# Kernel tuning notes

Measured on AMD Instinct MI355X. Metric: run time of the kernel, lower is better.

## Reference

```python
import jax, jax.numpy as jnp
import numpy as np

EPS = 1e-5

def conv3d(x, w):
    # x: [B,C,D,H,W], w: [O,I,3,3,3], stride 1, padding 1 (size preserving)
    return jax.lax.conv_general_dilated(
        x, w, window_strides=(1, 1, 1),
        padding=((1, 1), (1, 1), (1, 1)),
        dimension_numbers=('NCDHW', 'OIDHW', 'NCDHW'))

def deconv3d(x, w):
    # ConvTranspose3d(k=3, s=1, p=1) == conv3d with spatially flipped kernel, in/out swapped
    # torch ConvTranspose3d weight layout: [in, out, kD, kH, kW]
    wc = jnp.flip(w, axis=(2, 3, 4)).transpose(1, 0, 2, 3, 4)
    return conv3d(x, wc)

def batchnorm(x, bn):
    # bn: [4, C] rows = (gamma, beta, running_mean, running_var); inference mode
    g, b, m, v = bn[0], bn[1], bn[2], bn[3]
    scale = g * jax.lax.rsqrt(v + EPS)
    shift = b - m * scale
    return x * scale[None, :, None, None, None] + shift[None, :, None, None, None]

def qrnn_scan(Z, F, reverse):
    # gated linear recurrence h_t = f_t*h_{t-1} + (1-f_t)*z_t over depth axis (dim 2)
    Zs = jnp.moveaxis(Z, 2, 0)  # [D,B,C,H,W]
    Fs = jnp.moveaxis(F, 2, 0)
    def step(h, zf):
        z, f = zf
        h = f * h + (1.0 - f) * z
        return h, h
    h0 = jnp.zeros_like(Zs[0])  # h=None in torch == h=0 since f*0 vanishes
    _, hs = jax.lax.scan(step, h0, (Zs, Fs), reverse=reverse)
    return jnp.moveaxis(hs, 0, 2)

def qrnn_layer(x, w, bn, hidden, reverse, upsample, transpose):
    if upsample:
        # nn.Upsample(scale_factor=(1,2,2)) nearest
        x = jnp.repeat(jnp.repeat(x, 2, axis=3), 2, axis=4)
    g = deconv3d(x, w) if transpose else conv3d(x, w)
    g = batchnorm(g, bn)
    Z, F = g[:, :hidden], g[:, hidden:]
    return qrnn_scan(jnp.tanh(Z), jax.nn.sigmoid(F), reverse)

def setup_inputs():
    key = jax.random.key(0)
    ks = jax.random.split(key, 12)
    B, D = 4, 31
    x = jax.random.normal(ks[0], (B, 64, D, 32, 32), jnp.float32)
    xs2 = jax.random.normal(ks[1], (B, 32, D, 64, 64), jnp.float32)
    xs1 = jax.random.normal(ks[2], (B, 32, D, 64, 64), jnp.float32)
    xs0 = jax.random.normal(ks[3], (B, 16, D, 128, 128), jnp.float32)
    def wconv(k, shape):
        fan_in = shape[1] * 27
        return jax.random.normal(k, shape, jnp.float32) / np.float32(np.sqrt(fan_in))
    # layer0: UpsampleConv3d 64 -> 32 hidden (gates 64): Conv3d weight [64,64,3,3,3]
    w0 = wconv(ks[4], (64, 64, 3, 3, 3))
    # layer1: DeConv3D 32 -> 32 hidden (gates 64): ConvTranspose weight [in=32,out=64,3,3,3]
    w1 = wconv(ks[5], (32, 64, 3, 3, 3))
    # layer2: UpsampleConv3d 32 -> 16 hidden (gates 32): Conv3d weight [32,32,3,3,3]
    w2 = wconv(ks[6], (32, 32, 3, 3, 3))
    # layer3: DeConv3D 16 -> 16 hidden (gates 32): ConvTranspose weight [16,32,3,3,3]
    w3 = wconv(ks[7], (16, 32, 3, 3, 3))
    def mkbn(k, c):
        k1, k2, k3, k4 = jax.random.split(k, 4)
        return jnp.stack([
            jax.random.uniform(k1, (c,), jnp.float32, 0.5, 1.5),   # gamma
            jax.random.normal(k2, (c,), jnp.float32) * 0.1,        # beta
            jax.random.normal(k3, (c,), jnp.float32) * 0.1,        # running mean
            jax.random.uniform(k4, (c,), jnp.float32, 0.5, 1.5)])  # running var
    bn0 = mkbn(ks[8], 64)
    bn1 = mkbn(ks[9], 64)
    bn2 = mkbn(ks[10], 32)
    bn3 = mkbn(ks[11], 32)
    return dict(x=x, xs0=xs0, xs1=xs1, xs2=xs2,
                w0=w0, w1=w1, w2=w2, w3=w3,
                bn0=bn0, bn1=bn1, bn2=bn2, bn3=bn3)

def reference(x, xs0, xs1, xs2, w0, w1, w2, w3, bn0, bn1, bn2, bn3):
    # QRNN3DDecoder.forward with has_ad=True, reverse=False; scan direction alternates.
    # xs are popped last-first: xs2, xs1, xs0.
    h = qrnn_layer(x, w0, bn0, 32, False, True, False)          # upsample conv -> [B,32,D,64,64]
    h = qrnn_layer(h + xs2, w1, bn1, 32, True, False, True)     # deconv        -> [B,32,D,64,64]
    h = qrnn_layer(h + xs1, w2, bn2, 16, False, True, False)    # upsample conv -> [B,16,D,128,128]
    h = qrnn_layer(h + xs0, w3, bn3, 16, True, False, True)     # deconv        -> [B,16,D,128,128]
    return h
```

## Files before the change

### kernel.cpp

```cpp
#include <hip/hip_runtime.h>
#include <math.h>

#define BB 4
#define DD 31

typedef _Float16 half8 __attribute__((ext_vector_type(8)));
typedef float f32x4 __attribute__((ext_vector_type(4)));

__device__ __forceinline__ int swz(int b) { return b ^ (((b >> 7) & 7) << 4); }
__device__ __forceinline__ half8 ldswz(const _Float16* lin, int byteoff) {
    return *(const half8*)((const char*)lin + swz(byteoff));
}
__device__ __forceinline__ void stswz(_Float16* lin, int byteoff, half8 v) {
    *(half8*)((char*)lin + swz(byteoff)) = v;
}
__device__ __forceinline__ float fast_tanh(float y) {
    float e = __expf(2.f * y);
    return 1.f - 2.f * __builtin_amdgcn_rcpf(e + 1.f);
}
__device__ __forceinline__ float fast_sigmoid(float y) {
    return __builtin_amdgcn_rcpf(1.f + __expf(-y));
}


__global__ void bnprep(const float* __restrict__ bn, int C, float* __restrict__ sh) {
    int c = threadIdx.x;
    if (c >= C) return;
    float g = bn[c], b = bn[C + c], m = bn[2 * C + c], v = bn[3 * C + c];
    sh[c] = b - m * (g * rsqrtf(v + 1e-5f));
}

__global__ void wprepA(const float* __restrict__ src, const float* __restrict__ bn,
                       _Float16* __restrict__ dst, int CIN, int COUT, int KS, int tr) {
    int idx = blockIdx.x * 256 + threadIdx.x;
    int total = KS * 32 * COUT;
    if (idx >= total) return;
    int ki = idx % 32;
    int co = (idx / 32) % COUT;
    int ko = idx / (32 * COUT);
    int k = ko * 32 + ki;
    float v = 0.f;
    if (k < 27 * CIN) {
        int tap = k / CIN, ci = k % CIN;
        v = tr ? src[((size_t)ci * COUT + co) * 27 + (26 - tap)]
               : src[((size_t)co * CIN + ci) * 27 + tap];
        v *= bn[co] * rsqrtf(bn[3 * COUT + co] + 1e-5f);
    }
    dst[((size_t)ko * COUT + co) * 32 + ki] = (_Float16)v;
}

__global__ void wprepC(const float* __restrict__ src, const float* __restrict__ bn,
                       _Float16* __restrict__ dst, int CIN, int COUT, int KS, int tr) {
    int idx = blockIdx.x * 256 + threadIdx.x;
    int total = KS * 1024;
    if (idx >= total) return;
    int ki = idx & 31;
    int c16 = (idx >> 5) & 15;
    int n = (idx >> 9) & 1;
    int ko = idx >> 10;
    int co = n * (COUT / 2) + c16;
    int k = ko * 32 + ki;
    float v = 0.f;
    if (k < 27 * CIN) {
        int tap = k / CIN, ci = k % CIN;
        v = tr ? src[((size_t)ci * COUT + co) * 27 + (26 - tap)]
               : src[((size_t)co * CIN + ci) * 27 + tap];
        v *= bn[co] * rsqrtf(bn[3 * COUT + co] + 1e-5f);
    }
    dst[idx] = (_Float16)v;
}

__global__ void wprep_upA(const float* __restrict__ src, const float* __restrict__ bn,
                          _Float16* __restrict__ dst, int CIN, int COUT) {
    const int KS = 12 * CIN / 32;
    int idx = blockIdx.x * 256 + threadIdx.x;
    int total = 4 * KS * 32 * COUT;
    if (idx >= total) return;
    int ki = idx % 32;
    int co = (idx / 32) % COUT;
    int ko = (idx / (32 * COUT)) % KS;
    int par = idx / (32 * COUT * KS);
    int k = ko * 32 + ki;
    int ci = k % CIN, tap = k / CIN;
    int kd = tap >> 2, ih = (tap >> 1) & 1, iw = tap & 1;
    int ph = par >> 1, pw = par & 1;
    const float c[2][2][3] = {{{1, 0, 0}, {0, 1, 1}}, {{1, 1, 0}, {0, 0, 1}}};
    float v = 0.f;
    for (int kh = 0; kh < 3; ++kh)
        for (int kw = 0; kw < 3; ++kw)
            v += c[ph][ih][kh] * c[pw][iw][kw] *
                 src[((size_t)co * CIN + ci) * 27 + kd * 9 + kh * 3 + kw];
    v *= bn[co] * rsqrtf(bn[3 * COUT + co] + 1e-5f);
    dst[(((size_t)par * KS + ko) * COUT + co) * 32 + ki] = (_Float16)v;
}

__global__ void wprep_upB(const float* __restrict__ src, const float* __restrict__ bn,
                          _Float16* __restrict__ dst, int CIN, int COUT, int KS) {
    int idx = blockIdx.x * 256 + threadIdx.x;
    int total = 4 * KS * 1024;
    if (idx >= total) return;
    int ki = idx & 31;
    int c16 = (idx >> 5) & 15;
    int n = (idx >> 9) & 1;
    int ko = (idx >> 10) % KS;
    int par = idx / (KS * 1024);
    int co = n * (COUT / 2) + c16;
    int k = ko * 32 + ki;
    int ci = k % CIN, tap = k / CIN;
    int kd = tap >> 2, ih = (tap >> 1) & 1, iw = tap & 1;
    int ph = par >> 1, pw = par & 1;
    const float c[2][2][3] = {{{1, 0, 0}, {0, 1, 1}}, {{1, 1, 0}, {0, 0, 1}}};
    float v = 0.f;
    for (int kh = 0; kh < 3; ++kh)
        for (int kw = 0; kw < 3; ++kw)
            v += c[ph][ih][kh] * c[pw][iw][kw] *
                 src[((size_t)co * CIN + ci) * 27 + kd * 9 + kh * 3 + kw];
    v *= bn[co] * rsqrtf(bn[3 * COUT + co] + 1e-5f);
    dst[idx] = (_Float16)v;
}

__global__ __launch_bounds__(256) void xconv(const float* __restrict__ src,
                                             _Float16* __restrict__ dst) {
    int idx = blockIdx.x * 256 + threadIdx.x;
    if (idx >= 4 * 31 * 1024 * 8) return;
    int cb = idx & 7;
    int pos = (idx >> 3) & 1023;
    int bd = idx >> 13;
    int d = bd % 31, b = bd / 31;
    half8 v;
#pragma unroll
    for (int j = 0; j < 8; ++j)
        v[j] = (_Float16)src[(((size_t)b * 64 + cb * 8 + j) * 31 + d) * 1024 + pos];
    *(half8*)(dst + ((size_t)bd * 1024 + pos) * 64 + cb * 8) = v;
}

template <int C, int HW>
__global__ __launch_bounds__(256) void xst(const float* __restrict__ src,
                                           _Float16* __restrict__ dst) {
    int hw = blockIdx.x * 256 + threadIdx.x;
    int bd = blockIdx.y;
    int d = bd % DD, b = bd / DD;
    _Float16 tmp[C];
#pragma unroll
    for (int c = 0; c < C; ++c)
        tmp[c] = (_Float16)src[((size_t)(b * C + c) * DD + d) * HW + hw];
#pragma unroll
    for (int c8 = 0; c8 < C / 8; ++c8)
        *(half8*)(dst + ((size_t)bd * HW + hw) * C + c8 * 8) = *(half8*)(tmp + c8 * 8);
}

template <int CIN, int COUT, int S, int MINW>
__global__ __launch_bounds__(256, MINW) void conv_up(
    const _Float16* __restrict__ inp,
    const _Float16* __restrict__ wqu,
    const float* __restrict__ bnsh,
    _Float16* __restrict__ gout) {

    constexpr int SIN = S / 2;
    constexpr int KS = 12 * CIN / 32;
    constexpr int NCB = COUT / 16;
    constexpr int NC8 = CIN / 8;
    constexpr int IH = 6, IW = 18;
    constexpr int PATCH = 3 * IH * IW;

    __shared__ __align__(16) _Float16 lin[PATCH * CIN];

    const int tid = threadIdx.x;
    const int lane = tid & 63;
    const int wv = tid >> 6;
    const int col = lane & 15;
    const int grp = lane >> 4;
    const int ph = wv >> 1, pw = wv & 1;

    const int bwp = blockIdx.x * 16;
    const int bhp = blockIdx.y * 4;
    const int bz = blockIdx.z;
    const int d = bz % DD;

    for (int idx = tid; idx < PATCH * NC8; idx += 256) {
        int c8 = idx % NC8;
        int pos = idx / NC8;
        int iwp = pos % IW, t = pos / IW;
        int ihp = t % IH, kd = t / IH;
        int dz = d + kd - 1, gh = bhp - 1 + ihp, gw = bwp - 1 + iwp;
        half8 v = {0, 0, 0, 0, 0, 0, 0, 0};
        if ((unsigned)dz < (unsigned)DD && (unsigned)gh < (unsigned)SIN &&
            (unsigned)gw < (unsigned)SIN)
            v = *(const half8*)(inp +
                (((size_t)(bz + kd - 1) * SIN + gh) * SIN + gw) * CIN + c8 * 8);
        *(half8*)((char*)lin + swz((pos * CIN + c8 * 8) * 2)) = v;
    }
    __syncthreads();

    f32x4 acc[4][NCB];
#pragma unroll
    for (int f = 0; f < 4; ++f)
#pragma unroll
        for (int n = 0; n < NCB; ++n) acc[f][n] = {0.f, 0.f, 0.f, 0.f};

    const _Float16* wqp = wqu + (size_t)(ph * 2 + pw) * KS * COUT * 32;

#pragma unroll
    for (int ko = 0; ko < KS; ++ko) {
        int tap = (ko * 32) / CIN;
        int ci = (ko * 32) % CIN + grp * 8;
        int kd = tap >> 2, ih = (tap >> 1) & 1, iwk = tap & 1;

        int lcol = col + iwk + pw;
        int r0 = ih + ph;
        int cb = ((kd * IH + r0) * IW + lcol) * CIN + ci;
        half8 a[4];
#pragma unroll
        for (int f = 0; f < 4; ++f)
            a[f] = ldswz(lin, (cb + f * IW * CIN) * 2);

        half8 bfr[NCB];
#pragma unroll
        for (int n = 0; n < NCB; ++n)
            bfr[n] = *(const half8*)(wqp + ((ko * COUT + n * 16 + col) * 32 + grp * 8));
#pragma unroll
        for (int f = 0; f < 4; ++f)
#pragma unroll
            for (int n = 0; n < NCB; ++n)
                acc[f][n] = __builtin_amdgcn_mfma_f32_16x16x32_f16(a[f], bfr[n],
                                                                   acc[f][n], 0, 0, 0);
    }

    const size_t obase = (size_t)bz * S * S * COUT;
#pragma unroll
    for (int n = 0; n < NCB; ++n) {
        int co = n * 16 + col;
        float sh = bnsh[co];
#pragma unroll
        for (int f = 0; f < 4; ++f) {
            int h = 2 * (bhp + f) + ph;
#pragma unroll
            for (int r = 0; r < 4; ++r) {
                int w = 2 * (bwp + grp * 4 + r) + pw;
                float y = acc[f][n][r] + sh;
                float v = (n < NCB / 2) ? fast_tanh(y) : fast_sigmoid(y);
                gout[obase + ((size_t)h * S + w) * COUT + co] = (_Float16)v;
            }
        }
    }
}

template <int CIN, int COUT, int S, int KSTEPS>
__global__ __launch_bounds__(256, 2) void conv_mfma(
    const _Float16* __restrict__ inp,
    const _Float16* __restrict__ wq,
    const float* __restrict__ bnsh,
    _Float16* __restrict__ gout) {

    constexpr int IH = 18;
    constexpr int IW = 18;
    constexpr int NCB = COUT / 16;
    constexpr int NC8 = CIN / 8;
    constexpr int PATCH = 3 * IH * IW;

    __shared__ __align__(16) _Float16 lin[PATCH * CIN];

    const int tid = threadIdx.x;
    const int lane = tid & 63;
    const int wv = tid >> 6;
    const int col = lane & 15;
    const int grp = lane >> 4;

    const int w0 = blockIdx.x * 16;
    const int h0 = blockIdx.y * 16;
    const int bz = blockIdx.z;
    const int d = bz % DD;

    const int ibh = h0 - 1;
    const int ibw = w0 - 1;

    for (int idx = tid; idx < PATCH * NC8; idx += 256) {
        int c8 = idx % NC8;
        int pos = idx / NC8;
        int iw = pos % IW, t = pos / IW;
        int ih = t % IH, kd = t / IH;
        int dz = d + kd - 1, gh = ibh + ih, gw = ibw + iw;
        half8 v = {0, 0, 0, 0, 0, 0, 0, 0};
        if ((unsigned)dz < (unsigned)DD && (unsigned)gh < (unsigned)S &&
            (unsigned)gw < (unsigned)S)
            v = *(const half8*)(inp +
                (((size_t)(bz + kd - 1) * S + gh) * S + gw) * CIN + c8 * 8);
        *(half8*)((char*)lin + swz((pos * CIN + c8 * 8) * 2)) = v;
    }
    __syncthreads();

    f32x4 acc[4][NCB];
#pragma unroll
    for (int f = 0; f < 4; ++f)
#pragma unroll
        for (int n = 0; n < NCB; ++n) acc[f][n] = {0.f, 0.f, 0.f, 0.f};

#pragma unroll
    for (int ko = 0; ko < KSTEPS; ++ko) {
        int tap = (ko * 32) / CIN;
        int kd = tap / 9, kh = (tap / 3) % 3, kw = tap % 3;
        int ci = (ko * 32) % CIN + grp * 8;

        half8 a[4];
        int iw = col + kw;
        int cb = ((kd * IH + wv * 4 + kh) * IW + iw) * CIN + ci;
#pragma unroll
        for (int f = 0; f < 4; ++f)
            a[f] = ldswz(lin, (cb + f * IW * CIN) * 2);

        half8 bfr[NCB];
#pragma unroll
        for (int n = 0; n < NCB; ++n)
            bfr[n] = *(const half8*)(wq + ((ko * COUT + n * 16 + col) * 32 + grp * 8));
#pragma unroll
        for (int f = 0; f < 4; ++f)
#pragma unroll
            for (int n = 0; n < NCB; ++n)
                acc[f][n] = __builtin_amdgcn_mfma_f32_16x16x32_f16(a[f], bfr[n],
                                                                   acc[f][n], 0, 0, 0);
    }

    const size_t obase = (size_t)bz * S * S * COUT;
#pragma unroll
    for (int n = 0; n < NCB; ++n) {
        int co = n * 16 + col;
        float sh = bnsh[co];
#pragma unroll
        for (int f = 0; f < 4; ++f) {
            int h = h0 + wv * 4 + f;
#pragma unroll
            for (int r = 0; r < 4; ++r) {
                int w = w0 + grp * 4 + r;
                float y = acc[f][n][r] + sh;
                float v = (n < NCB / 2) ? fast_tanh(y) : fast_sigmoid(y);
                gout[obase + ((size_t)h * S + w) * COUT + co] = (_Float16)v;
            }
        }
    }
}

template <int H, int HW>
__global__ __launch_bounds__(256) void qscan(
    const _Float16* __restrict__ g, const float* __restrict__ xs,
    _Float16* __restrict__ hout, int rev) {
    constexpr int NCB = H / 8;
    int idx = blockIdx.x * 256 + threadIdx.x;
    if (idx >= BB * HW * NCB) return;
    int cb = idx % NCB;
    int hw = (idx / NCB) % HW;
    int b = idx / (NCB * HW);
    int c0 = cb * 8;

    float h[8];
#pragma unroll
    for (int j = 0; j < 8; ++j) h[j] = 0.f;

    for (int t = 0; t < DD; ++t) {
        int d = rev ? (DD - 1 - t) : t;
        const _Float16* gp = g + ((size_t)(b * DD + d) * HW + hw) * (2 * H);
        half8 z8 = *(const half8*)(gp + c0);
        half8 f8 = *(const half8*)(gp + H + c0);
        half8 o;
#pragma unroll
        for (int j = 0; j < 8; ++j) {
            float fv = (float)f8[j];
            h[j] = fv * h[j] + (1.f - fv) * (float)z8[j];
            o[j] = (_Float16)(h[j] + xs[(((size_t)b * H + c0 + j) * DD + d) * HW + hw]);
        }
        *(half8*)(hout + ((size_t)(b * DD + d) * HW + hw) * H + c0) = o;
    }
}

template <int CIN, int S, int HID, int KS, int REV, int LAST>
__global__ __launch_bounds__(256, 2) void fconv_up1(
    const _Float16* __restrict__ inp,
    const _Float16* __restrict__ wq,
    const float* __restrict__ bnsh,
    const _Float16* __restrict__ xs,
    _Float16* __restrict__ hout,
    float* __restrict__ fout) {

    constexpr int SIN = S / 2;
    constexpr int IW = 18;
    constexpr int IHP = 6;
    constexpr int NC8 = CIN / 8;
    constexpr int P8 = IHP * IW * NC8;
    constexpr int NST = (P8 + 255) / 256;
    constexpr int PLANEB = IHP * IW * CIN * 2;
    constexpr int LWB = 3 * PLANEB;
    constexpr int WH = KS * 1024;

    __shared__ __align__(16) _Float16 lds[(LWB / 2) + WH];

    const int tid = threadIdx.x;
    const int lane = tid & 63;
    const int wv = tid >> 6;
    const int col = lane & 15;
    const int grp = lane >> 4;

    const int bwp = blockIdx.x * 16;
    const int bhp = blockIdx.y * 4;
    const int par = blockIdx.z & 3;
    const int b = blockIdx.z >> 2;
    const int ph = par >> 1, pw = par & 1;
    const size_t bbase = (size_t)b * DD;

    const float shz = bnsh[col];
    const float shf = bnsh[HID + col];
    const int hc = col;
    const _Float16* wqb = wq + (size_t)par * KS * 1024;

    auto stage_now = [&](int dz) {
        int slot = (dz + 33) % 3;
        for (int idx = tid; idx < P8; idx += 256) {
            int c8 = idx % NC8;
            int pos = idx / NC8;
            int ih = pos / IW, iw = pos % IW;
            int gh = bhp - 1 + ih, gw = bwp - 1 + iw;
            half8 v = {0, 0, 0, 0, 0, 0, 0, 0};
            if ((unsigned)dz < (unsigned)DD && (unsigned)gh < (unsigned)SIN &&
                (unsigned)gw < (unsigned)SIN)
                v = *(const half8*)(inp + (((bbase + dz) * SIN + gh) * SIN + gw) * CIN + c8 * 8);
            stswz(lds, slot * PLANEB + (pos * CIN + c8 * 8) * 2, v);
        }
    };

    constexpr int dir = REV ? -1 : 1;
    const int d0 = REV ? DD - 1 : 0;
    stage_now(d0 - dir);
    stage_now(d0);
    stage_now(d0 + dir);
    for (int i = tid; i < WH / 8; i += 256) {
        half8 v = *(const half8*)(wqb + i * 8);
        stswz(lds, LWB + i * 16, v);
    }
    __syncthreads();

    float hst[4];
#pragma unroll
    for (int r = 0; r < 4; ++r) hst[r] = 0.f;

    for (int t = 0; t < DD; ++t) {
        const int d = d0 + dir * t;
        const int dzl = d + 2 * dir;
        const int sm = (d - 1 + 33) % 3;
        const int s0 = (d + 33) % 3;
        const int sp = (d + 1 + 33) % 3;
        const int scommit = REV ? sp : sm;

        half8 sv[NST];
#pragma unroll
        for (int i = 0; i < NST; ++i) {
            int idx = tid + i * 256;
            half8 v = {0, 0, 0, 0, 0, 0, 0, 0};
            if (idx < P8) {
                int c8 = idx % NC8;
                int pos = idx / NC8;
                int ih = pos / IW, iw = pos % IW;
                int gh = bhp - 1 + ih, gw = bwp - 1 + iw;
                if ((unsigned)dzl < (unsigned)DD && (unsigned)gh < (unsigned)SIN &&
                    (unsigned)gw < (unsigned)SIN)
                    v = *(const half8*)(inp +
                        (((bbase + dzl) * SIN + gh) * SIN + gw) * CIN + c8 * 8);
            }
            sv[i] = v;
        }

        f32x4 accz = {0.f, 0.f, 0.f, 0.f};
        f32x4 accf = {0.f, 0.f, 0.f, 0.f};
#pragma unroll
        for (int ko = 0; ko < KS; ++ko) {
            int tap = (ko * 32) / CIN;
            int ci = (ko * 32) % CIN + grp * 8;
            int kd = tap >> 2, ihh = (tap >> 1) & 1, iwk = tap & 1;
            int slot = kd == 0 ? sm : (kd == 1 ? s0 : sp);
            int lcol = col + iwk + pw;
            int row = wv + ihh + ph;
            half8 a = ldswz(lds, slot * PLANEB + ((row * IW + lcol) * CIN + ci) * 2);
            half8 bf0 = ldswz(lds, LWB + (ko * 1024 + col * 32 + grp * 8) * 2);
            half8 bf1 = ldswz(lds, LWB + (ko * 1024 + 512 + col * 32 + grp * 8) * 2);
            accz = __builtin_amdgcn_mfma_f32_16x16x32_f16(a, bf0, accz, 0, 0, 0);
            accf = __builtin_amdgcn_mfma_f32_16x16x32_f16(a, bf1, accf, 0, 0, 0);
        }

        __syncthreads();
#pragma unroll
        for (int i = 0; i < NST; ++i) {
            int idx = tid + i * 256;
            if (idx < P8) {
                int c8 = idx % NC8;
                int pos = idx / NC8;
                stswz(lds, scommit * PLANEB + (pos * CIN + c8 * 8) * 2, sv[i]);
            }
        }

        int h = 2 * (bhp + wv) + ph;
#pragma unroll
        for (int r = 0; r < 4; ++r) {
            int w = 2 * (bwp + grp * 4 + r) + pw;
            size_t sp2 = (size_t)h * S + w;
            float z = fast_tanh(accz[r] + shz);
            float fg = fast_sigmoid(accf[r] + shf);
            hst[r] = fg * hst[r] + (1.f - fg) * z;
            if (LAST) {
                fout[(((size_t)b * HID + hc) * DD + d) * ((size_t)S * S) + sp2] = hst[r];
            } else {
                float xv = (float)xs[((bbase + d) * ((size_t)S * S) + sp2) * HID + hc];
                hout[((bbase + d) * ((size_t)S * S) + sp2) * HID + hc] =
                    (_Float16)(hst[r] + xv);
            }
        }
        __syncthreads();
    }
}

template <int CIN, int S, int HID, int KS, int NF, int REV>
__global__ __launch_bounds__(256, 2) void fconv3(
    const _Float16* __restrict__ inp,
    const _Float16* __restrict__ wq,
    const float* __restrict__ bnsh,
    float* __restrict__ fout) {

    constexpr int IW = 18;
    constexpr int TH = 4 * NF;
    constexpr int IHP = TH + 2;
    constexpr int NC8 = CIN / 8;
    constexpr int P8 = IHP * IW * NC8;
    constexpr int NST = (P8 + 255) / 256;
    constexpr int PLANEB = IHP * IW * CIN * 2;
    constexpr int LWB = 3 * PLANEB;
    constexpr int WH = KS * 1024;

    __shared__ __align__(16) _Float16 lds[(LWB / 2) + WH];

    const int tid = threadIdx.x;
    const int lane = tid & 63;
    const int wv = tid >> 6;
    const int col = lane & 15;
    const int grp = lane >> 4;

    const int w0 = blockIdx.x * 16;
    const int h0 = blockIdx.y * TH;
    const int b = blockIdx.z;
    const size_t bbase = (size_t)b * DD;

    const float shz = bnsh[col];
    const float shf = bnsh[HID + col];
    const int hc = col;

    auto stage_now = [&](int dz) {
        int slot = (dz + 33) % 3;
        for (int idx = tid; idx < P8; idx += 256) {
            int c8 = idx % NC8;
            int pos = idx / NC8;
            int ih = pos / IW, iw = pos % IW;
            int gh = h0 - 1 + ih, gw = w0 - 1 + iw;
            half8 v = {0, 0, 0, 0, 0, 0, 0, 0};
            if ((unsigned)dz < (unsigned)DD && (unsigned)gh < (unsigned)S &&
                (unsigned)gw < (unsigned)S)
                v = *(const half8*)(inp + (((bbase + dz) * S + gh) * S + gw) * CIN + c8 * 8);
            stswz(lds, slot * PLANEB + (pos * CIN + c8 * 8) * 2, v);
        }
    };

    constexpr int dir = REV ? -1 : 1;
    const int d0 = REV ? DD - 1 : 0;
    stage_now(d0 - dir);
    stage_now(d0);
    stage_now(d0 + dir);
    for (int i = tid; i < WH / 8; i += 256) {
        half8 v = *(const half8*)(wq + i * 8);
        stswz(lds, LWB + i * 16, v);
    }
    __syncthreads();

    float hst[NF][4];
#pragma unroll
    for (int f = 0; f < NF; ++f)
#pragma unroll
        for (int r = 0; r < 4; ++r) hst[f][r] = 0.f;

    for (int t = 0; t < DD; ++t) {
        const int d = d0 + dir * t;
        const int dzl = d + 2 * dir;
        const int sm = (d - 1 + 33) % 3;
        const int s0 = (d + 33) % 3;
        const int sp = (d + 1 + 33) % 3;
        const int scommit = REV ? sp : sm;

        half8 sv[NST];
#pragma unroll
        for (int i = 0; i < NST; ++i) {
            int idx = tid + i * 256;
            half8 v = {0, 0, 0, 0, 0, 0, 0, 0};
            if (idx < P8) {
                int c8 = idx % NC8;
                int pos = idx / NC8;
                int ih = pos / IW, iw = pos % IW;
                int gh = h0 - 1 + ih, gw = w0 - 1 + iw;
                if ((unsigned)dzl < (unsigned)DD && (unsigned)gh < (unsigned)S &&
                    (unsigned)gw < (unsigned)S)
                    v = *(const half8*)(inp +
                        (((bbase + dzl) * S + gh) * S + gw) * CIN + c8 * 8);
            }
            sv[i] = v;
        }

        f32x4 acc[NF][2];
#pragma unroll
        for (int f = 0; f < NF; ++f) {
            acc[f][0] = {0.f, 0.f, 0.f, 0.f};
            acc[f][1] = {0.f, 0.f, 0.f, 0.f};
        }
#pragma unroll
        for (int ko = 0; ko < KS; ++ko) {
            int kd, kh, kw, ci;
            if (CIN >= 32) {
                int tap = (ko * 32) / CIN;
                kd = tap / 9; kh = (tap / 3) % 3; kw = tap % 3;
                ci = (ko * 32) % CIN + grp * 8;
            } else {
                int t0 = (2 * ko < 27) ? 2 * ko : 26;
                int t1 = (2 * ko + 1 < 27) ? 2 * ko + 1 : 26;
                int hi = grp >> 1;
                kd = hi ? t1 / 9 : t0 / 9;
                kh = hi ? (t1 / 3) % 3 : (t0 / 3) % 3;
                kw = hi ? t1 % 3 : t0 % 3;
                ci = (grp & 1) * 8;
            }
            int slot = kd == 0 ? sm : (kd == 1 ? s0 : sp);
            int iw = col + kw;
            half8 a[NF];
#pragma unroll
            for (int f = 0; f < NF; ++f)
                a[f] = ldswz(lds, slot * PLANEB +
                             (((wv * NF + f + kh) * IW + iw) * CIN + ci) * 2);
            half8 bf0 = ldswz(lds, LWB + (ko * 1024 + col * 32 + grp * 8) * 2);
            half8 bf1 = ldswz(lds, LWB + (ko * 1024 + 512 + col * 32 + grp * 8) * 2);
#pragma unroll
            for (int f = 0; f < NF; ++f) {
                acc[f][0] = __builtin_amdgcn_mfma_f32_16x16x32_f16(a[f], bf0, acc[f][0], 0, 0, 0);
                acc[f][1] = __builtin_amdgcn_mfma_f32_16x16x32_f16(a[f], bf1, acc[f][1], 0, 0, 0);
            }
        }

        __syncthreads();
#pragma unroll
        for (int i = 0; i < NST; ++i) {
            int idx = tid + i * 256;
            if (idx < P8) {
                int c8 = idx % NC8;
                int pos = idx / NC8;
                stswz(lds, scommit * PLANEB + (pos * CIN + c8 * 8) * 2, sv[i]);
            }
        }

#pragma unroll
        for (int f = 0; f < NF; ++f) {
            int h = h0 + wv * NF + f;
#pragma unroll
            for (int r = 0; r < 4; ++r) {
                int w = w0 + grp * 4 + r;
                size_t sp2 = (size_t)h * S + w;
                float z = fast_tanh(acc[f][0][r] + shz);
                float fg = fast_sigmoid(acc[f][1][r] + shf);
                hst[f][r] = fg * hst[f][r] + (1.f - fg) * z;
                fout[(((size_t)b * HID + hc) * DD + d) * ((size_t)S * S) + sp2] = hst[f][r];
            }
        }
        __syncthreads();
    }
}

extern "C" void kernel_launch(void* const* d_in, const int* in_sizes, int n_in,
                              void* d_out, int out_size, void* d_ws, size_t ws_size,
                              hipStream_t stream) {
    const float* x   = (const float*)d_in[0];
    const float* xs0 = (const float*)d_in[1];
    const float* xs1 = (const float*)d_in[2];
    const float* xs2 = (const float*)d_in[3];
    const float* w0  = (const float*)d_in[4];
    const float* w1  = (const float*)d_in[5];
    const float* w2  = (const float*)d_in[6];
    const float* w3  = (const float*)d_in[7];
    const float* bn0 = (const float*)d_in[8];
    const float* bn1 = (const float*)d_in[9];
    const float* bn2 = (const float*)d_in[10];
    const float* bn3 = (const float*)d_in[11];
    float* out = (float*)d_out;

    char* p = (char*)d_ws;
    _Float16* xf   = (_Float16*)p; p += (size_t)124 * 1024 * 64 * 2;
    _Float16* gA   = (_Float16*)p; p += (size_t)124 * 4096 * 64 * 2;
    _Float16* hA   = (_Float16*)p; p += (size_t)124 * 4096 * 32 * 2;
    _Float16* hA2  = (_Float16*)p; p += (size_t)124 * 4096 * 32 * 2;
    _Float16* hB   = (_Float16*)p; p += (size_t)124 * 16384 * 16 * 2;
    _Float16* xs0f = (_Float16*)p; p += (size_t)124 * 16384 * 16 * 2;
    _Float16* wq0u = (_Float16*)p; p += (size_t)4 * 24 * 64 * 32 * 2;
    _Float16* wq1  = (_Float16*)p; p += (size_t)27 * 64 * 32 * 2;
    _Float16* wq2u = (_Float16*)p; p += (size_t)4 * 12 * 1024 * 2;
    _Float16* wq3  = (_Float16*)p; p += (size_t)14 * 1024 * 2;
    float* sh0 = (float*)p; p += 64 * 4;
    float* sh1 = (float*)p; p += 64 * 4;
    float* sh2 = (float*)p; p += 64 * 4;
    float* sh3 = (float*)p; p += 64 * 4;

    xconv<<<(4 * 31 * 1024 * 8 + 255) / 256, 256, 0, stream>>>(x, xf);
    xst<16, 16384><<<dim3(64, BB * DD), 256, 0, stream>>>(xs0, xs0f);
    wprep_upA<<<(4 * 24 * 32 * 64 + 255) / 256, 256, 0, stream>>>(w0, bn0, wq0u, 64, 64);
    wprepA<<<(27 * 32 * 64 + 255) / 256, 256, 0, stream>>>(w1, bn1, wq1, 32, 64, 27, 1);
    wprep_upB<<<(4 * 12 * 1024 + 255) / 256, 256, 0, stream>>>(w2, bn2, wq2u, 32, 32, 12);
    wprepC<<<(14 * 1024 + 255) / 256, 256, 0, stream>>>(w3, bn3, wq3, 16, 32, 14, 1);
    bnprep<<<1, 64, 0, stream>>>(bn0, 64, sh0);
    bnprep<<<1, 64, 0, stream>>>(bn1, 64, sh1);
    bnprep<<<1, 64, 0, stream>>>(bn2, 32, sh2);
    bnprep<<<1, 64, 0, stream>>>(bn3, 32, sh3);

    conv_up<64, 64, 64, 3><<<dim3(2, 8, BB * DD), 256, 0, stream>>>(xf, wq0u, sh0, gA);
    qscan<32, 4096><<<(BB * 4096 * 4 + 255) / 256, 256, 0, stream>>>(gA, xs2, hA, 0);

    conv_mfma<32, 64, 64, 27><<<dim3(4, 4, BB * DD), 256, 0, stream>>>(hA, wq1, sh1, gA);
    qscan<32, 4096><<<(BB * 4096 * 4 + 255) / 256, 256, 0, stream>>>(gA, xs1, hA2, 1);

    fconv_up1<32, 128, 16, 12, 0, 0><<<dim3(4, 16, BB * 4), 256, 0, stream>>>(
        hA2, wq2u, sh2, xs0f, hB, nullptr);

    fconv3<16, 128, 16, 14, 2, 1><<<dim3(8, 16, BB), 256, 0, stream>>>(
        hB, wq3, sh3, out);
}
```

Baseline: 510.2 us.

## Store layer-2 output and xs0 in parity-blocked layout for coalesced writes

Changes the intermediate hB buffer and the converted xs0f buffer to a parity-split layout: each depth slice is stored as four 64x64 sub-planes indexed by (h&1, w&1). fconv_up1 then writes each parity block's outputs contiguously instead of with stride-2 scatter, and reads the xs0 skip input the same way. fconv3 gathers its input through a matching address function. The aim is more coalesced stores and loads in the upsample kernel, at the cost of less contiguous halo gathers in the final conv and the removal of the unused LAST path.

```diff
diff --git a/kernel.cpp b/kernel.cpp
--- a/kernel.cpp
+++ b/kernel.cpp
@@ -134,28 +134,27 @@
     *(half8*)(dst + ((size_t)bd * 1024 + pos) * 64 + cb * 8) = v;
 }
 
-template <int C, int HW>
-__global__ __launch_bounds__(256) void xst(const float* __restrict__ src,
-                                           _Float16* __restrict__ dst) {
+__global__ __launch_bounds__(256) void xst_pb(const float* __restrict__ src,
+                                              _Float16* __restrict__ dst) {
     int hw = blockIdx.x * 256 + threadIdx.x;
     int bd = blockIdx.y;
     int d = bd % DD, b = bd / DD;
-    _Float16 tmp[C];
-#pragma unroll
-    for (int c = 0; c < C; ++c)
-        tmp[c] = (_Float16)src[((size_t)(b * C + c) * DD + d) * HW + hw];
-#pragma unroll
-    for (int c8 = 0; c8 < C / 8; ++c8)
-        *(half8*)(dst + ((size_t)bd * HW + hw) * C + c8 * 8) = *(half8*)(tmp + c8 * 8);
+    int h = hw >> 7, w = hw & 127;
+    int par = (h & 1) * 2 + (w & 1);
+    int p = (h >> 1) * 64 + (w >> 1);
+    _Float16 tmp[16];
+#pragma unroll
+    for (int c = 0; c < 16; ++c)
+        tmp[c] = (_Float16)src[((size_t)(b * 16 + c) * DD + d) * 16384 + hw];
+    _Float16* o = dst + (((size_t)bd * 4 + par) * 4096 + p) * 16;
+    *(half8*)o = *(half8*)tmp;
+    *(half8*)(o + 8) = *(half8*)(tmp + 8);
 }
 
 template <int CIN, int COUT, int S, int MINW>
 __global__ __launch_bounds__(256, MINW) void conv_up(
-    const _Float16* __restrict__ inp,
-    const _Float16* __restrict__ wqu,
-    const float* __restrict__ bnsh,
-    _Float16* __restrict__ gout) {
-
+    const _Float16* __restrict__ inp, const _Float16* __restrict__ wqu,
+    const float* __restrict__ bnsh, _Float16* __restrict__ gout) {
     constexpr int SIN = S / 2;
     constexpr int KS = 12 * CIN / 32;
     constexpr int NCB = COUT / 16;
@@ -247,11 +246,8 @@
 
 template <int CIN, int COUT, int S, int KSTEPS>
 __global__ __launch_bounds__(256, 2) void conv_mfma(
-    const _Float16* __restrict__ inp,
-    const _Float16* __restrict__ wq,
-    const float* __restrict__ bnsh,
-    _Float16* __restrict__ gout) {
-
+    const _Float16* __restrict__ inp, const _Float16* __restrict__ wq,
+    const float* __restrict__ bnsh, _Float16* __restrict__ gout) {
     constexpr int IH = 18;
     constexpr int IW = 18;
     constexpr int NCB = COUT / 16;
@@ -371,14 +367,13 @@
     }
 }
 
-template <int CIN, int S, int HID, int KS, int REV, int LAST>
+template <int CIN, int S, int HID, int KS, int REV>
 __global__ __launch_bounds__(256, 2) void fconv_up1(
     const _Float16* __restrict__ inp,
     const _Float16* __restrict__ wq,
     const float* __restrict__ bnsh,
     const _Float16* __restrict__ xs,
-    _Float16* __restrict__ hout,
-    float* __restrict__ fout) {
+    _Float16* __restrict__ hout) {
 
     constexpr int SIN = S / 2;
     constexpr int IW = 18;
@@ -402,7 +397,6 @@
     const int bhp = blockIdx.y * 4;
     const int par = blockIdx.z & 3;
     const int b = blockIdx.z >> 2;
-    const int ph = par >> 1, pw = par & 1;
     const size_t bbase = (size_t)b * DD;
 
     const float shz = bnsh[col];
@@ -440,6 +434,9 @@
 #pragma unroll
     for (int r = 0; r < 4; ++r) hst[r] = 0.f;
 
+    const int ph = par >> 1, pw = par & 1;
+    (void)ph; (void)pw;
+
     for (int t = 0; t < DD; ++t) {
         const int d = d0 + dir * t;
         const int dzl = d + 2 * dir;
@@ -494,21 +491,17 @@
             }
         }
 
-        int h = 2 * (bhp + wv) + ph;
+        const size_t pb = ((bbase + d) * 4 + par) * (size_t)(SIN * SIN);
+        const int hp = bhp + wv;
 #pragma unroll
         for (int r = 0; r < 4; ++r) {
-            int w = 2 * (bwp + grp * 4 + r) + pw;
-            size_t sp2 = (size_t)h * S + w;
+            int wp = bwp + grp * 4 + r;
+            size_t sp2 = pb + hp * SIN + wp;
             float z = fast_tanh(accz[r] + shz);
             float fg = fast_sigmoid(accf[r] + shf);
             hst[r] = fg * hst[r] + (1.f - fg) * z;
-            if (LAST) {
-                fout[(((size_t)b * HID + hc) * DD + d) * ((size_t)S * S) + sp2] = hst[r];
-            } else {
-                float xv = (float)xs[((bbase + d) * ((size_t)S * S) + sp2) * HID + hc];
-                hout[((bbase + d) * ((size_t)S * S) + sp2) * HID + hc] =
-                    (_Float16)(hst[r] + xv);
-            }
+            float xv = (float)xs[sp2 * HID + hc];
+            hout[sp2 * HID + hc] = (_Float16)(hst[r] + xv);
         }
         __syncthreads();
     }
@@ -530,6 +523,7 @@
     constexpr int PLANEB = IHP * IW * CIN * 2;
     constexpr int LWB = 3 * PLANEB;
     constexpr int WH = KS * 1024;
+    constexpr int SIN = S / 2;
 
     __shared__ __align__(16) _Float16 lds[(LWB / 2) + WH];
 
@@ -547,6 +541,11 @@
     const float shz = bnsh[col];
     const float shf = bnsh[HID + col];
     const int hc = col;
+
+    auto gaddr = [&](int dz, int gh, int gw) -> size_t {
+        return ((((bbase + dz) * 2 + (gh & 1)) * 2 + (gw & 1)) * (size_t)(SIN * SIN) +
+                (gh >> 1) * SIN + (gw >> 1)) * CIN;
+    };
 
     auto stage_now = [&](int dz) {
         int slot = (dz + 33) % 3;
@@ -558,7 +557,7 @@
             half8 v = {0, 0, 0, 0, 0, 0, 0, 0};
             if ((unsigned)dz < (unsigned)DD && (unsigned)gh < (unsigned)S &&
                 (unsigned)gw < (unsigned)S)
-                v = *(const half8*)(inp + (((bbase + dz) * S + gh) * S + gw) * CIN + c8 * 8);
+                v = *(const half8*)(inp + gaddr(dz, gh, gw) + c8 * 8);
             stswz(lds, slot * PLANEB + (pos * CIN + c8 * 8) * 2, v);
         }
     };
@@ -600,8 +599,7 @@
                 int gh = h0 - 1 + ih, gw = w0 - 1 + iw;
                 if ((unsigned)dzl < (unsigned)DD && (unsigned)gh < (unsigned)S &&
                     (unsigned)gw < (unsigned)S)
-                    v = *(const half8*)(inp +
-                        (((bbase + dzl) * S + gh) * S + gw) * CIN + c8 * 8);
+                    v = *(const half8*)(inp + gaddr(dzl, gh, gw) + c8 * 8);
             }
             sv[i] = v;
         }
@@ -706,7 +704,7 @@
     float* sh3 = (float*)p; p += 64 * 4;
 
     xconv<<<(4 * 31 * 1024 * 8 + 255) / 256, 256, 0, stream>>>(x, xf);
-    xst<16, 16384><<<dim3(64, BB * DD), 256, 0, stream>>>(xs0, xs0f);
+    xst_pb<<<dim3(64, BB * DD), 256, 0, stream>>>(xs0, xs0f);
     wprep_upA<<<(4 * 24 * 32 * 64 + 255) / 256, 256, 0, stream>>>(w0, bn0, wq0u, 64, 64);
     wprepA<<<(27 * 32 * 64 + 255) / 256, 256, 0, stream>>>(w1, bn1, wq1, 32, 64, 27, 1);
     wprep_upB<<<(4 * 12 * 1024 + 255) / 256, 256, 0, stream>>>(w2, bn2, wq2u, 32, 32, 12);
@@ -722,8 +720,8 @@
     conv_mfma<32, 64, 64, 27><<<dim3(4, 4, BB * DD), 256, 0, stream>>>(hA, wq1, sh1, gA);
     qscan<32, 4096><<<(BB * 4096 * 4 + 255) / 256, 256, 0, stream>>>(gA, xs1, hA2, 1);
 
-    fconv_up1<32, 128, 16, 12, 0, 0><<<dim3(4, 16, BB * 4), 256, 0, stream>>>(
-        hA2, wq2u, sh2, xs0f, hB, nullptr);
+    fconv_up1<32, 128, 16, 12, 0><<<dim3(4, 16, BB * 4), 256, 0, stream>>>(
+        hA2, wq2u, sh2, xs0f, hB);
 
     fconv3<16, 128, 16, 14, 2, 1><<<dim3(8, 16, BB), 256, 0, stream>>>(
         hB, wq3, sh3, out);
```

New measurement: 510.0 us. No clear change (-0.0%).
